# Kernel optimization log

Measured on AMD Instinct MI355X. Metric: run time of the kernel, lower is better.

The kernel has to match this reference:

```python
import jax, jax.numpy as jnp
import numpy as np
from math import sqrt

N_IN = 1024
N_OUT = 1024
DEPTH = 10
N_NODES = 2 ** (DEPTH + 1) - 1  # 2047
BATCH = 32768


def setup_inputs() -> dict:
    key = jax.random.key(0)
    k1, k2, k3 = jax.random.split(key, 3)
    f1 = 1.0 / sqrt(N_IN)
    f2 = 1.0 / sqrt(DEPTH + 1)
    x = jax.random.normal(k1, (BATCH, N_IN), dtype=jnp.float32)
    w1s = jax.random.uniform(k2, (N_NODES, N_IN), dtype=jnp.float32, minval=-f1, maxval=f1)
    w2s = jax.random.uniform(k3, (N_NODES, N_OUT), dtype=jnp.float32, minval=-f2, maxval=f2)
    return {"x": x, "w1s": w1s, "w2s": w2s, "depth": DEPTH}


def reference(x, w1s, w2s, depth):
    batch = x.shape[0]

    def step(current_node, _):
        # current_node: [b] int32 node index at this tree level
        plane_score = jnp.einsum('bi,bi->b', x, w1s[current_node])  # [b]
        plane_choice = (plane_score > 0).astype(jnp.int32)
        next_node = current_node * 2 + plane_choice + 1
        return next_node, (current_node, plane_score)

    node0 = jnp.zeros((batch,), dtype=jnp.int32)
    _, (all_nodes, all_scores) = jax.lax.scan(step, node0, None, length=depth + 1)
    all_nodes = all_nodes.T    # [b, depth+1]
    all_scores = all_scores.T  # [b, depth+1]

    selected_w2s = w2s[all_nodes]  # [b, depth+1, nOut]
    y = jnp.einsum('bij,bi->bj', selected_w2s, all_scores)
    return y
```

## Files before the change

kernel.cpp:

```cpp
#include <hip/hip_runtime.h>


typedef float        f32x4 __attribute__((ext_vector_type(4)));
typedef unsigned int u32x4 __attribute__((ext_vector_type(4)));

#define FFF_BATCH  32768
#define FFF_NIN    1024
#define FFF_NOUT   1024
#define FFF_LEVELS 11
#define FFF_NODES  2047
#define FFF_EPS    0.035f

__device__ __forceinline__ f32x4 ld_nt4f(const f32x4* p) { return __builtin_nontemporal_load(p); }
__device__ __forceinline__ float ub(unsigned d, int k) {
    return (float)((d >> (8 * k)) & 0xffu);
}

__device__ __forceinline__ int sdot4(unsigned a, unsigned b, int c) {
#if __has_builtin(__builtin_amdgcn_sdot4)
    return __builtin_amdgcn_sdot4((int)a, (int)b, c, false);
#else
#pragma unroll
    for (int k = 0; k < 4; ++k) {
        const int ai = (int)(a << (24 - 8 * k)) >> 24;
        const int bi = (int)(b << (24 - 8 * k)) >> 24;
        c += ai * bi;
    }
    return c;
#endif
}

template<int CTRL>
__device__ __forceinline__ float dpp_add(float v) {
    const int t = __builtin_amdgcn_update_dpp(0, __float_as_int(v), CTRL, 0xF, 0xF, true);
    return v + __int_as_float(t);
}
__device__ __forceinline__ float wave_sum(float v) {
    v = dpp_add<0x111>(v); v = dpp_add<0x112>(v);
    v = dpp_add<0x114>(v); v = dpp_add<0x118>(v);
    v = dpp_add<0x142>(v); v = dpp_add<0x143>(v);
    return __int_as_float(__builtin_amdgcn_readlane(__float_as_int(v), 63));
}
template<int CTRL>
__device__ __forceinline__ int dpp_addi(int v) {
    return v + __builtin_amdgcn_update_dpp(0, v, CTRL, 0xF, 0xF, true);
}
__device__ __forceinline__ int wave_sum_i(int v) {
    v = dpp_addi<0x111>(v); v = dpp_addi<0x112>(v);
    v = dpp_addi<0x114>(v); v = dpp_addi<0x118>(v);
    v = dpp_addi<0x142>(v); v = dpp_addi<0x143>(v);
    return __builtin_amdgcn_readlane(v, 63);
}
template<int CTRL>
__device__ __forceinline__ float dpp_max(float v) {
    const int t = __builtin_amdgcn_update_dpp(0, __float_as_int(v), CTRL, 0xF, 0xF, true);
    return fmaxf(v, __int_as_float(t));
}
__device__ __forceinline__ float wave_max(float v) {
    v = dpp_max<0x111>(v); v = dpp_max<0x112>(v);
    v = dpp_max<0x114>(v); v = dpp_max<0x118>(v);
    v = dpp_max<0x142>(v); v = dpp_max<0x143>(v);
    return __int_as_float(__builtin_amdgcn_readlane(__float_as_int(v), 63));
}

__global__ void fff_quant_u8(const float* __restrict__ w1, const float* __restrict__ w2,
                             unsigned char* __restrict__ q1, unsigned char* __restrict__ q2,
                             float* __restrict__ s1, float* __restrict__ s2)
{
    const int node = blockIdx.x;
    const int t    = threadIdx.x;
    const int wave = t >> 6;
    const int lane = t & 63;

    const f32x4* r1 = reinterpret_cast<const f32x4*>(w1 + (size_t)node * FFF_NIN);
    const f32x4* r2 = reinterpret_cast<const f32x4*>(w2 + (size_t)node * FFF_NOUT);
    const int si = 64 * (t & 3) + (t >> 2);
    const f32x4 v1 = r1[si];
    const f32x4 v2 = r2[si];

    float m1 = 0.f, m2 = 0.f;
#pragma unroll
    for (int k = 0; k < 4; ++k) {
        m1 = fmaxf(m1, fabsf(v1[k]));
        m2 = fmaxf(m2, fabsf(v2[k]));
    }
#pragma unroll
    for (int m = 1; m < 64; m <<= 1) {
        m1 = fmaxf(m1, __shfl_xor(m1, m, 64));
        m2 = fmaxf(m2, __shfl_xor(m2, m, 64));
    }
    __shared__ float sm1[4], sm2[4];
    if (lane == 0) { sm1[wave] = m1; sm2[wave] = m2; }
    __syncthreads();
    m1 = fmaxf(fmaxf(sm1[0], sm1[1]), fmaxf(sm1[2], sm1[3]));
    m2 = fmaxf(fmaxf(sm2[0], sm2[1]), fmaxf(sm2[2], sm2[3]));

    const float st1 = (m1 > 0.f) ? m1 / 127.f : 1.f;
    const float st2 = (m2 > 0.f) ? m2 / 127.f : 1.f;
    if (t == 0) { s1[node] = st1; s2[node] = st2; }

    unsigned d1 = 0, d2 = 0;
#pragma unroll
    for (int k = 0; k < 4; ++k) {
        const int i1 = (int)rintf(v1[k] / st1);
        const int u2 = (int)rintf(v2[k] / st2) + 128;
        d1 |= ((unsigned)i1 & 0xffu) << (8 * k);
        d2 |= ((unsigned)u2 & 0xffu) << (8 * k);
    }
    reinterpret_cast<unsigned*>(q1)[(size_t)node * 256 + t] = d1;
    reinterpret_cast<unsigned*>(q2)[(size_t)node * 256 + t] = d2;
}

__global__ __launch_bounds__(256, 8) void fff_main_u8(
    const float*         __restrict__ x,
    const unsigned char* __restrict__ q1,
    const float*         __restrict__ s1,
    const float*         __restrict__ w1f,
    const unsigned char* __restrict__ q2,
    const float*         __restrict__ s2,
    float*               __restrict__ y)
{
    const int row  = blockIdx.x * 4 + (threadIdx.x >> 6);
    const int lane = threadIdx.x & 63;

    const f32x4* x4 = reinterpret_cast<const f32x4*>(x + (size_t)row * FFF_NIN);
    f32x4 xv[4];
#pragma unroll
    for (int c = 0; c < 4; ++c) xv[c] = ld_nt4f(&x4[c * 64 + lane]);

    float mx = 0.f;
#pragma unroll
    for (int c = 0; c < 4; ++c)
#pragma unroll
        for (int k = 0; k < 4; ++k) mx = fmaxf(mx, fabsf(xv[c][k]));
    mx = wave_max(mx);
    const float stx = (mx > 0.f) ? mx / 127.f : 1.f;
    const float inv = (mx > 0.f) ? 127.f / mx : 0.f;

    unsigned xq[4];
#pragma unroll
    for (int c = 0; c < 4; ++c) {
        const int a0 = (int)rintf(xv[c][0] * inv);
        const int a1 = (int)rintf(xv[c][1] * inv);
        const int a2 = (int)rintf(xv[c][2] * inv);
        const int a3 = (int)rintf(xv[c][3] * inv);
        xq[c] = ((unsigned)a0 & 0xffu) | (((unsigned)a1 & 0xffu) << 8) |
                (((unsigned)a2 & 0xffu) << 16) | (((unsigned)a3 & 0xffu) << 24);
    }

    f32x4 acc[4];
#pragma unroll
    for (int c = 0; c < 4; ++c) acc[c] = (f32x4)(0.f);
    float corr = 0.f;

    const u32x4* q1v = reinterpret_cast<const u32x4*>(q1);
    const u32x4* q2v = reinterpret_cast<const u32x4*>(q2);

    int node = 0;
    u32x4 d1 = q1v[lane];
    u32x4 d2 = q2v[lane];
    float sc1 = s1[0];
    float sc2 = s2[0];

#pragma unroll 1
    for (int l = 0; l < FFF_LEVELS; ++l) {
        int idot = 0;
#pragma unroll
        for (int c = 0; c < 4; ++c) idot = sdot4(xq[c], d1[c], idot);

        float p = (float)wave_sum_i(idot) * (stx * sc1);

        if (__builtin_expect(fabsf(p) < FFF_EPS, 0)) {
            const f32x4* w14 = reinterpret_cast<const f32x4*>(w1f + (size_t)node * FFF_NIN);
            float s = 0.f;
#pragma unroll
            for (int c = 0; c < 4; ++c) {
                const f32x4 w = w14[c * 64 + lane];
                s = fmaf(xv[c][0], w[0], s);
                s = fmaf(xv[c][1], w[1], s);
                s = fmaf(xv[c][2], w[2], s);
                s = fmaf(xv[c][3], w[3], s);
            }
            p = wave_sum(s);
        }

        const int next = 2 * node + 1 + ((p > 0.f) ? 1 : 0);
        u32x4 nd1 = d1, nd2 = d2;
        float ns1 = sc1, ns2 = sc2;
        if (l < FFF_LEVELS - 1) {
            const int un = __builtin_amdgcn_readfirstlane(next);
            nd1 = q1v[(size_t)un * 64 + lane];
            nd2 = q2v[(size_t)un * 64 + lane];
            ns1 = s1[un];
            ns2 = s2[un];
        }

        const float s2l = p * sc2;
        corr = fmaf(s2l, 128.f, corr);
#pragma unroll
        for (int c = 0; c < 4; ++c) {
#pragma unroll
            for (int k = 0; k < 4; ++k)
                acc[c][k] = fmaf(s2l, ub(d2[c], k), acc[c][k]);
        }

        node = next;
        d1 = nd1; d2 = nd2; sc1 = ns1; sc2 = ns2;
    }

    f32x4* y4 = reinterpret_cast<f32x4*>(y + (size_t)row * FFF_NOUT);
#pragma unroll
    for (int c = 0; c < 4; ++c) {
        f32x4 o;
        o[0] = acc[c][0] - corr; o[1] = acc[c][1] - corr;
        o[2] = acc[c][2] - corr; o[3] = acc[c][3] - corr;
        __builtin_nontemporal_store(o, &y4[c * 64 + lane]);
    }
}

__global__ __launch_bounds__(256, 4) void fff_fused_f32(
    const float* __restrict__ x, const float* __restrict__ w1s,
    const float* __restrict__ w2s, float* __restrict__ y)
{
    const int row  = blockIdx.x * 4 + (threadIdx.x >> 6);
    const int lane = threadIdx.x & 63;
    const f32x4* x4 = reinterpret_cast<const f32x4*>(x + (size_t)row * FFF_NIN);
    f32x4 xv[4];
#pragma unroll
    for (int c = 0; c < 4; ++c) xv[c] = x4[c * 64 + lane];
    f32x4 acc[4];
#pragma unroll
    for (int c = 0; c < 4; ++c) acc[c] = (f32x4)(0.f);
    int node = 0;
#pragma unroll 1
    for (int l = 0; l < FFF_LEVELS; ++l) {
        const f32x4* w14 = reinterpret_cast<const f32x4*>(w1s + (size_t)node * FFF_NIN);
        const f32x4* w24 = reinterpret_cast<const f32x4*>(w2s + (size_t)node * FFF_NOUT);
        f32x4 wv[4], uv[4];
#pragma unroll
        for (int c = 0; c < 4; ++c) { wv[c] = w14[c * 64 + lane]; uv[c] = w24[c * 64 + lane]; }
        float p = 0.f;
#pragma unroll
        for (int c = 0; c < 4; ++c) {
            p = fmaf(xv[c][0], wv[c][0], p); p = fmaf(xv[c][1], wv[c][1], p);
            p = fmaf(xv[c][2], wv[c][2], p); p = fmaf(xv[c][3], wv[c][3], p);
        }
#pragma unroll
        for (int m = 1; m < 64; m <<= 1) p += __shfl_xor(p, m, 64);
#pragma unroll
        for (int c = 0; c < 4; ++c) {
            acc[c][0] = fmaf(p, uv[c][0], acc[c][0]); acc[c][1] = fmaf(p, uv[c][1], acc[c][1]);
            acc[c][2] = fmaf(p, uv[c][2], acc[c][2]); acc[c][3] = fmaf(p, uv[c][3], acc[c][3]);
        }
        node = node * 2 + 1 + ((p > 0.f) ? 1 : 0);
    }
    f32x4* y4 = reinterpret_cast<f32x4*>(y + (size_t)row * FFF_NOUT);
#pragma unroll
    for (int c = 0; c < 4; ++c) y4[c * 64 + lane] = acc[c];
}

extern "C" void kernel_launch(void* const* d_in, const int* in_sizes, int n_in,
                              void* d_out, int out_size, void* d_ws, size_t ws_size,
                              hipStream_t stream) {
    const float* x   = (const float*)d_in[0];
    const float* w1s = (const float*)d_in[1];
    const float* w2s = (const float*)d_in[2];
    float* y = (float*)d_out;

    const size_t sc_bytes = 8192;
    const size_t q_bytes  = (size_t)FFF_NODES * 1024;
    const size_t need = 2 * sc_bytes + 2 * q_bytes;

    if (ws_size >= need) {
        float* s1 = (float*)d_ws;
        float* s2 = (float*)((char*)d_ws + sc_bytes);
        unsigned char* q1 = (unsigned char*)d_ws + 2 * sc_bytes;
        unsigned char* q2 = q1 + q_bytes;
        fff_quant_u8<<<FFF_NODES, 256, 0, stream>>>(w1s, w2s, q1, q2, s1, s2);
        fff_main_u8<<<FFF_BATCH / 4, 256, 0, stream>>>(x, q1, s1, w1s, q2, s2, y);
    } else {
        fff_fused_f32<<<FFF_BATCH / 4, 256, 0, stream>>>(x, w1s, w2s, y);
    }
}
```

Before: 82.63 us.

## Interleave per-node quantized weights and scales, shrink blocks, drop fp32 x registers

Packs each node's quantized w1 and w2 rows next to each other in one 2 KB record and merges the two scales into a float2, so each tree step fetches from one contiguous region. The main kernel drops to 128 threads (2 rows) per block, and it no longer keeps the fp32 x vector in registers after quantizing; the rare fallback path reloads x from memory instead. The aim is fewer scattered loads per step and lower register pressure for higher occupancy. The cost is extra global traffic when the near-zero fallback fires.

```diff
diff --git a/kernel.cpp b/kernel.cpp
--- a/kernel.cpp
+++ b/kernel.cpp
@@ -64,8 +64,7 @@
 }
 
 __global__ void fff_quant_u8(const float* __restrict__ w1, const float* __restrict__ w2,
-                             unsigned char* __restrict__ q1, unsigned char* __restrict__ q2,
-                             float* __restrict__ s1, float* __restrict__ s2)
+                             unsigned char* __restrict__ q, float2* __restrict__ sc)
 {
     const int node = blockIdx.x;
     const int t    = threadIdx.x;
@@ -97,7 +96,7 @@
 
     const float st1 = (m1 > 0.f) ? m1 / 127.f : 1.f;
     const float st2 = (m2 > 0.f) ? m2 / 127.f : 1.f;
-    if (t == 0) { s1[node] = st1; s2[node] = st2; }
+    if (t == 0) sc[node] = make_float2(st1, st2);
 
     unsigned d1 = 0, d2 = 0;
 #pragma unroll
@@ -107,45 +106,45 @@
         d1 |= ((unsigned)i1 & 0xffu) << (8 * k);
         d2 |= ((unsigned)u2 & 0xffu) << (8 * k);
     }
-    reinterpret_cast<unsigned*>(q1)[(size_t)node * 256 + t] = d1;
-    reinterpret_cast<unsigned*>(q2)[(size_t)node * 256 + t] = d2;
-}
-
-__global__ __launch_bounds__(256, 8) void fff_main_u8(
+    unsigned* qw = reinterpret_cast<unsigned*>(q + (size_t)node * 2048);
+    qw[t]       = d1;
+    qw[256 + t] = d2;
+}
+
+__global__ __launch_bounds__(128, 8) void fff_main_u8(
     const float*         __restrict__ x,
-    const unsigned char* __restrict__ q1,
-    const float*         __restrict__ s1,
+    const unsigned char* __restrict__ q,
+    const float2*        __restrict__ sc,
     const float*         __restrict__ w1f,
-    const unsigned char* __restrict__ q2,
-    const float*         __restrict__ s2,
     float*               __restrict__ y)
 {
-    const int row  = blockIdx.x * 4 + (threadIdx.x >> 6);
+    const int row  = blockIdx.x * 2 + (threadIdx.x >> 6);
     const int lane = threadIdx.x & 63;
 
     const f32x4* x4 = reinterpret_cast<const f32x4*>(x + (size_t)row * FFF_NIN);
-    f32x4 xv[4];
-#pragma unroll
-    for (int c = 0; c < 4; ++c) xv[c] = ld_nt4f(&x4[c * 64 + lane]);
-
-    float mx = 0.f;
-#pragma unroll
-    for (int c = 0; c < 4; ++c)
-#pragma unroll
-        for (int k = 0; k < 4; ++k) mx = fmaxf(mx, fabsf(xv[c][k]));
-    mx = wave_max(mx);
-    const float stx = (mx > 0.f) ? mx / 127.f : 1.f;
-    const float inv = (mx > 0.f) ? 127.f / mx : 0.f;
 
     unsigned xq[4];
-#pragma unroll
-    for (int c = 0; c < 4; ++c) {
-        const int a0 = (int)rintf(xv[c][0] * inv);
-        const int a1 = (int)rintf(xv[c][1] * inv);
-        const int a2 = (int)rintf(xv[c][2] * inv);
-        const int a3 = (int)rintf(xv[c][3] * inv);
-        xq[c] = ((unsigned)a0 & 0xffu) | (((unsigned)a1 & 0xffu) << 8) |
-                (((unsigned)a2 & 0xffu) << 16) | (((unsigned)a3 & 0xffu) << 24);
+    float stx;
+    {
+        f32x4 xv[4];
+#pragma unroll
+        for (int c = 0; c < 4; ++c) xv[c] = ld_nt4f(&x4[c * 64 + lane]);
+        float mx = 0.f;
+#pragma unroll
+        for (int c = 0; c < 4; ++c)
+#pragma unroll
+            for (int k = 0; k < 4; ++k) mx = fmaxf(mx, fabsf(xv[c][k]));
+        mx = wave_max(mx);
+        stx = (mx > 0.f) ? mx / 127.f : 1.f;
+        const float inv = (mx > 0.f) ? 127.f / mx : 0.f;
+#pragma unroll
+        for (int c = 0; c < 4; ++c) {
+            unsigned pk = 0;
+#pragma unroll
+            for (int k = 0; k < 4; ++k)
+                pk |= ((unsigned)(int)rintf(xv[c][k] * inv) & 0xffu) << (8 * k);
+            xq[c] = pk;
+        }
     }
 
     f32x4 acc[4];
@@ -153,14 +152,11 @@
     for (int c = 0; c < 4; ++c) acc[c] = (f32x4)(0.f);
     float corr = 0.f;
 
-    const u32x4* q1v = reinterpret_cast<const u32x4*>(q1);
-    const u32x4* q2v = reinterpret_cast<const u32x4*>(q2);
-
     int node = 0;
-    u32x4 d1 = q1v[lane];
-    u32x4 d2 = q2v[lane];
-    float sc1 = s1[0];
-    float sc2 = s2[0];
+    const unsigned char* nb = q;
+    u32x4 d1 = *reinterpret_cast<const u32x4*>(nb + lane * 16);
+    u32x4 d2 = *reinterpret_cast<const u32x4*>(nb + 1024 + lane * 16);
+    float2 s12 = sc[0];
 
 #pragma unroll 1
     for (int l = 0; l < FFF_LEVELS; ++l) {
@@ -168,34 +164,35 @@
 #pragma unroll
         for (int c = 0; c < 4; ++c) idot = sdot4(xq[c], d1[c], idot);
 
-        float p = (float)wave_sum_i(idot) * (stx * sc1);
+        float p = (float)wave_sum_i(idot) * (stx * s12.x);
 
         if (__builtin_expect(fabsf(p) < FFF_EPS, 0)) {
             const f32x4* w14 = reinterpret_cast<const f32x4*>(w1f + (size_t)node * FFF_NIN);
             float s = 0.f;
 #pragma unroll
             for (int c = 0; c < 4; ++c) {
-                const f32x4 w = w14[c * 64 + lane];
-                s = fmaf(xv[c][0], w[0], s);
-                s = fmaf(xv[c][1], w[1], s);
-                s = fmaf(xv[c][2], w[2], s);
-                s = fmaf(xv[c][3], w[3], s);
+                const f32x4 xc = ld_nt4f(&x4[c * 64 + lane]);
+                const f32x4 w  = w14[c * 64 + lane];
+                s = fmaf(xc[0], w[0], s);
+                s = fmaf(xc[1], w[1], s);
+                s = fmaf(xc[2], w[2], s);
+                s = fmaf(xc[3], w[3], s);
             }
             p = wave_sum(s);
         }
 
         const int next = 2 * node + 1 + ((p > 0.f) ? 1 : 0);
         u32x4 nd1 = d1, nd2 = d2;
-        float ns1 = sc1, ns2 = sc2;
+        float2 ns12 = s12;
         if (l < FFF_LEVELS - 1) {
             const int un = __builtin_amdgcn_readfirstlane(next);
-            nd1 = q1v[(size_t)un * 64 + lane];
-            nd2 = q2v[(size_t)un * 64 + lane];
-            ns1 = s1[un];
-            ns2 = s2[un];
-        }
-
-        const float s2l = p * sc2;
+            const unsigned char* b2 = q + (size_t)un * 2048;
+            nd1  = *reinterpret_cast<const u32x4*>(b2 + lane * 16);
+            nd2  = *reinterpret_cast<const u32x4*>(b2 + 1024 + lane * 16);
+            ns12 = sc[un];
+        }
+
+        const float s2l = p * s12.y;
         corr = fmaf(s2l, 128.f, corr);
 #pragma unroll
         for (int c = 0; c < 4; ++c) {
@@ -205,7 +202,7 @@
         }
 
         node = next;
-        d1 = nd1; d2 = nd2; sc1 = ns1; sc2 = ns2;
+        d1 = nd1; d2 = nd2; s12 = ns12;
     }
 
     f32x4* y4 = reinterpret_cast<f32x4*>(y + (size_t)row * FFF_NOUT);
@@ -267,17 +264,15 @@
     const float* w2s = (const float*)d_in[2];
     float* y = (float*)d_out;
 
-    const size_t sc_bytes = 8192;
-    const size_t q_bytes  = (size_t)FFF_NODES * 1024;
-    const size_t need = 2 * sc_bytes + 2 * q_bytes;
+    const size_t sc_bytes = 16384;
+    const size_t q_bytes  = (size_t)FFF_NODES * 2048;
+    const size_t need = sc_bytes + q_bytes;
 
     if (ws_size >= need) {
-        float* s1 = (float*)d_ws;
-        float* s2 = (float*)((char*)d_ws + sc_bytes);
-        unsigned char* q1 = (unsigned char*)d_ws + 2 * sc_bytes;
-        unsigned char* q2 = q1 + q_bytes;
-        fff_quant_u8<<<FFF_NODES, 256, 0, stream>>>(w1s, w2s, q1, q2, s1, s2);
-        fff_main_u8<<<FFF_BATCH / 4, 256, 0, stream>>>(x, q1, s1, w1s, q2, s2, y);
+        float2* scp = (float2*)d_ws;
+        unsigned char* q = (unsigned char*)d_ws + sc_bytes;
+        fff_quant_u8<<<FFF_NODES, 256, 0, stream>>>(w1s, w2s, q, scp);
+        fff_main_u8<<<FFF_BATCH / 2, 128, 0, stream>>>(x, q, scp, w1s, y);
     } else {
         fff_fused_f32<<<FFF_BATCH / 4, 256, 0, stream>>>(x, w1s, w2s, y);
     }
```

Result: slower. 102.6 us (+24.2%).
